# Optimization experiments

Hardware: AMD Instinct MI355X
Metric: run time of the kernel (lower is better)

The kernel has to match this reference:

```python
import jax, jax.numpy as jnp
import numpy as np

B, C, H, W = 4, 256, 48, 48
NH = 4                 # num_heads
HD = C // NH           # head_dim = 64
KD = HD // 2           # key_dim = 32 (attn_ratio=0.5)
QKV_C = C + 2 * KD * NH  # 512
FF = 2 * C             # 512
EPS = 1e-3             # ultralytics BatchNorm2d eps


def _bn(x, g, b, m, v):
    # eval-mode BatchNorm2d over channel dim 1 of NCHW
    s = g / jnp.sqrt(v + EPS)
    return x * s[:, None, None] + (b - m * s)[:, None, None]


def _conv1x1(x, w):
    # w: [out_c, in_c]
    return jnp.einsum('bchw,oc->bohw', x, w)


def _dwconv3x3(x, w):
    # depthwise 3x3, padding 1; w: [C, 1, 3, 3]
    return jax.lax.conv_general_dilated(
        x, w, (1, 1), [(1, 1), (1, 1)],
        dimension_numbers=('NCHW', 'OIHW', 'NCHW'),
        feature_group_count=C)


def setup_inputs() -> dict:
    key = jax.random.key(0)
    ks = jax.random.split(key, 32)
    d = {}
    d['x'] = jax.random.normal(ks[0], (B, C, H, W), dtype=jnp.float32)

    def bn_params(i, ch):
        g = 0.5 + jax.random.uniform(ks[i], (ch,), dtype=jnp.float32)
        b = 0.1 * jax.random.normal(ks[i + 1], (ch,), dtype=jnp.float32)
        m = 0.1 * jax.random.normal(ks[i + 2], (ch,), dtype=jnp.float32)
        v = 0.5 + jax.random.uniform(ks[i + 3], (ch,), dtype=jnp.float32)
        return g, b, m, v

    d['qkv_w'] = 0.05 * jax.random.normal(ks[1], (QKV_C, C), dtype=jnp.float32)
    d['qkv_g'], d['qkv_b'], d['qkv_m'], d['qkv_v'] = bn_params(2, QKV_C)
    d['pe_w'] = 0.1 * jax.random.normal(ks[6], (C, 1, 3, 3), dtype=jnp.float32)
    d['pe_g'], d['pe_b'], d['pe_m'], d['pe_v'] = bn_params(7, C)
    d['proj_w'] = 0.05 * jax.random.normal(ks[11], (C, C), dtype=jnp.float32)
    d['proj_g'], d['proj_b'], d['proj_m'], d['proj_v'] = bn_params(12, C)
    d['f1_w'] = 0.05 * jax.random.normal(ks[16], (FF, C), dtype=jnp.float32)
    d['f1_g'], d['f1_b'], d['f1_m'], d['f1_v'] = bn_params(17, FF)
    d['f2_w'] = 0.05 * jax.random.normal(ks[21], (C, FF), dtype=jnp.float32)
    d['f2_g'], d['f2_b'], d['f2_m'], d['f2_v'] = bn_params(22, C)
    return d


def reference(x, qkv_w, qkv_g, qkv_b, qkv_m, qkv_v,
              pe_w, pe_g, pe_b, pe_m, pe_v,
              proj_w, proj_g, proj_b, proj_m, proj_v,
              f1_w, f1_g, f1_b, f1_m, f1_v,
              f2_w, f2_g, f2_b, f2_m, f2_v):
    b, c, h, w = x.shape
    n = h * w
    # --- Attention ---
    qkv = _bn(_conv1x1(x, qkv_w), qkv_g, qkv_b, qkv_m, qkv_v)
    qkv = qkv.reshape(b, NH, 2 * KD + HD, n)
    q = qkv[:, :, :KD]            # [b, nh, kd, n]
    k = qkv[:, :, KD:2 * KD]      # [b, nh, kd, n]
    v = qkv[:, :, 2 * KD:]        # [b, nh, hd, n]
    attn = jnp.einsum('bhkn,bhkm->bhnm', q, k) * (KD ** -0.5)
    attn = jax.nn.softmax(attn, axis=-1)
    o = jnp.einsum('bhdm,bhnm->bhdn', v, attn).reshape(b, c, h, w)
    pe = _bn(_dwconv3x3(v.reshape(b, c, h, w), pe_w), pe_g, pe_b, pe_m, pe_v)
    attn_out = _bn(_conv1x1(o + pe, proj_w), proj_g, proj_b, proj_m, proj_v)
    x = x + attn_out  # shortcut
    # --- FFN ---
    f = _conv1x1(x, f1_w)
    f = _bn(f, f1_g, f1_b, f1_m, f1_v)
    f = f * jax.nn.sigmoid(f)  # SiLU
    f = _bn(_conv1x1(f, f2_w), f2_g, f2_b, f2_m, f2_v)
    return x + f  # shortcut
```

## Files before the change

kernel.cpp:

```cpp
#include <hip/hip_runtime.h>
#include <math.h>

#define Bb   4
#define Cc   256
#define Hh   48
#define Ww   48
#define NNp  2304
#define Rr   9216
#define NHd  4
#define QKVC 512
#define EPSf 1e-3f

typedef unsigned int   u32;
typedef unsigned short u16;
typedef __attribute__((ext_vector_type(8))) __bf16 bf16x8;
typedef __attribute__((ext_vector_type(4))) float  f32x4;

#if __has_builtin(__builtin_amdgcn_exp2f)
#define EXP2F(x) __builtin_amdgcn_exp2f(x)
#else
#define EXP2F(x) __expf((x) * 0.6931471805599453f)
#endif

__device__ __forceinline__ u16 f2bf(float f) {
    u32 u = __float_as_uint(f);
    u = (u + 0x7fffu + ((u >> 16) & 1u)) >> 16;
    return (u16)u;
}
__device__ __forceinline__ float bf2f(u16 h) {
    return __uint_as_float((u32)h << 16);
}
__device__ __forceinline__ u32 pk2bf(float a, float b) {
    union { __bf16 h; u16 u; } ua, ub;
    ua.h = (__bf16)a; ub.h = (__bf16)b;
    return (u32)ua.u | ((u32)ub.u << 16);
}
__device__ __forceinline__ void gload16(const void* gsrc, void* ldst) {
    __builtin_amdgcn_global_load_lds(
        (const __attribute__((address_space(1))) u32*)gsrc,
        (__attribute__((address_space(3))) u32*)ldst, 16, 0, 0);
}

__global__ __launch_bounds__(64)
void prep_all(const float* __restrict__ W0, const float* __restrict__ g0, const float* __restrict__ b0, const float* __restrict__ m0, const float* __restrict__ v0, u16* __restrict__ Wb0, float* __restrict__ bi0,
              const float* __restrict__ W1, const float* __restrict__ g1, const float* __restrict__ b1, const float* __restrict__ m1, const float* __restrict__ v1, u16* __restrict__ Wb1, float* __restrict__ bi1,
              const float* __restrict__ W2, const float* __restrict__ g2, const float* __restrict__ b2, const float* __restrict__ m2, const float* __restrict__ v2, u16* __restrict__ Wb2, float* __restrict__ bi2,
              const float* __restrict__ W3, const float* __restrict__ g3, const float* __restrict__ b3, const float* __restrict__ m3, const float* __restrict__ v3, u16* __restrict__ Wb3, float* __restrict__ bi3)
{
    const int bid = blockIdx.x;
    const float *W, *gp, *bp, *mp, *vp;
    u16* Wb; float* bias;
    int K = 256, oc;
    float c = 1.f;
    if (bid < 512) {
        oc = bid; W = W0; gp = g0; bp = b0; mp = m0; vp = v0; Wb = Wb0; bias = bi0;
        if ((oc & 127) < 32) c = 0.17677669529663687f * 1.4426950408889634f;
    } else if (bid < 768) {
        oc = bid - 512; W = W1; gp = g1; bp = b1; mp = m1; vp = v1; Wb = Wb1; bias = bi1;
    } else if (bid < 1280) {
        oc = bid - 768; W = W2; gp = g2; bp = b2; mp = m2; vp = v2; Wb = Wb2; bias = bi2;
    } else {
        oc = bid - 1280; W = W3; gp = g3; bp = b3; mp = m3; vp = v3; Wb = Wb3; bias = bi3;
        K = 512;
    }
    const int lane = threadIdx.x;
    const float s = gp[oc] * rsqrtf(vp[oc] + EPSf);
    if (lane == 0) bias[oc] = (bp[oc] - mp[oc] * s) * c;
    const float sc = s * c;
    for (int k0 = lane * 4; k0 < K; k0 += 256) {
        const float4 w = *(const float4*)(W + (size_t)oc * K + k0);
        u32 lo = (u32)f2bf(w.x * sc) | ((u32)f2bf(w.y * sc) << 16);
        u32 hi = (u32)f2bf(w.z * sc) | ((u32)f2bf(w.w * sc) << 16);
        *(uint2*)(Wb + (size_t)oc * K + k0) = make_uint2(lo, hi);
    }
}

__global__ __launch_bounds__(256)
void cvt_x(const float* __restrict__ x, u16* __restrict__ Xt)
{
    const int b = blockIdx.z, c0 = blockIdx.y * 64, n0 = blockIdx.x * 64;
    __shared__ float tile[64][65];
    const int tid = threadIdx.x;
    {
        const int n = tid & 63, cl = tid >> 6;
        #pragma unroll
        for (int cc = 0; cc < 16; ++cc) {
            const int c = cc * 4 + cl;
            tile[c][n] = x[((size_t)b * Cc + c0 + c) * NNp + n0 + n];
        }
    }
    __syncthreads();
    {
        const int n = tid >> 2, q = tid & 3;
        #pragma unroll
        for (int j = 0; j < 2; ++j) {
            const int ch = q * 2 + j, c = ch * 8;
            u32 w[4];
            #pragma unroll
            for (int e = 0; e < 4; ++e)
                w[e] = (u32)f2bf(tile[c + 2*e][n]) | ((u32)f2bf(tile[c + 2*e + 1][n]) << 16);
            *(uint4*)(Xt + ((size_t)b * NNp + n0 + n) * Cc + c0 + c)
                = make_uint4(w[0], w[1], w[2], w[3]);
        }
    }
}

template<int BN_, int FN_, int MODE>
__global__ __launch_bounds__(256)
void gemm_mfma(const u16* __restrict__ A, const u16* __restrict__ Bx,
               const float* __restrict__ bias, const float* __restrict__ resid,
               float* __restrict__ Yf, u16* __restrict__ Yt, int M, int K)
{
    constexpr int WN = FN_ * 16;
    const int r0 = blockIdx.x * BN_;
    const int m0 = blockIdx.y * 128;
    const int tid = threadIdx.x;
    const int lane = tid & 63, wid = tid >> 6;
    const int g = lane >> 4, i16 = lane & 15;
    const int wr = wid >> 1, wc = wid & 1;

    __shared__ __align__(16) u16 Al[2][4][128][8];
    __shared__ __align__(16) u16 Bl[2][4][BN_][8];

    f32x4 acc[4][FN_];
    #pragma unroll
    for (int i = 0; i < 4; ++i)
        #pragma unroll
        for (int j = 0; j < FN_; ++j) acc[i][j] = (f32x4){0.f, 0.f, 0.f, 0.f};

    #pragma unroll
    for (int ii = 0; ii < 2; ++ii) {
        const int ci = ii * 256 + tid;
        gload16(A + (size_t)(m0 + (ci & 127)) * K + (ci >> 7) * 8,
                (u16*)&Al[0][0][0][0] + (size_t)ci * 8);
    }
    if (BN_ == 128) {
        #pragma unroll
        for (int ii = 0; ii < 2; ++ii) {
            const int ci = ii * 256 + tid;
            gload16(Bx + (size_t)(r0 + (ci & 127)) * K + (ci >> 7) * 8,
                    (u16*)&Bl[0][0][0][0] + (size_t)ci * 8);
        }
    } else {
        gload16(Bx + (size_t)(r0 + (tid & 63)) * K + (tid >> 6) * 8,
                (u16*)&Bl[0][0][0][0] + (size_t)tid * 8);
    }
    __syncthreads();

    int buf = 0;
    for (int k0 = 0; k0 < K; k0 += 32) {
        if (k0 + 32 < K) {
            const int kn = k0 + 32;
            #pragma unroll
            for (int ii = 0; ii < 2; ++ii) {
                const int ci = ii * 256 + tid;
                gload16(A + (size_t)(m0 + (ci & 127)) * K + kn + (ci >> 7) * 8,
                        (u16*)&Al[buf ^ 1][0][0][0] + (size_t)ci * 8);
            }
            if (BN_ == 128) {
                #pragma unroll
                for (int ii = 0; ii < 2; ++ii) {
                    const int ci = ii * 256 + tid;
                    gload16(Bx + (size_t)(r0 + (ci & 127)) * K + kn + (ci >> 7) * 8,
                            (u16*)&Bl[buf ^ 1][0][0][0] + (size_t)ci * 8);
                }
            } else {
                gload16(Bx + (size_t)(r0 + (tid & 63)) * K + kn + (tid >> 6) * 8,
                        (u16*)&Bl[buf ^ 1][0][0][0] + (size_t)tid * 8);
            }
        }
        bf16x8 af[4], bf[FN_];
        #pragma unroll
        for (int ao = 0; ao < 4; ++ao)
            af[ao] = *(const bf16x8*)&Al[buf][g][wr * 64 + ao * 16 + i16][0];
        #pragma unroll
        for (int bo = 0; bo < FN_; ++bo)
            bf[bo] = *(const bf16x8*)&Bl[buf][g][wc * WN + bo * 16 + i16][0];
        __builtin_amdgcn_s_setprio(1);
        #pragma unroll
        for (int ao = 0; ao < 4; ++ao)
            #pragma unroll
            for (int bo = 0; bo < FN_; ++bo)
                acc[ao][bo] = __builtin_amdgcn_mfma_f32_16x16x32_bf16(
                    af[ao], bf[bo], acc[ao][bo], 0, 0, 0);
        __builtin_amdgcn_s_setprio(0);
        __syncthreads();
        buf ^= 1;
    }

    const int b  = r0 / NNp;
    const int nb = r0 - b * NNp;
    #pragma unroll
    for (int ao = 0; ao < 4; ++ao) {
        const int oc0 = m0 + wr * 64 + ao * 16 + g * 4;
        const float4 t4 = *(const float4*)(bias + oc0);
        #pragma unroll
        for (int bo = 0; bo < FN_; ++bo) {
            const int nloc = wc * WN + bo * 16 + i16;
            float y[4];
            y[0] = acc[ao][bo][0] + t4.x;  y[1] = acc[ao][bo][1] + t4.y;
            y[2] = acc[ao][bo][2] + t4.z;  y[3] = acc[ao][bo][3] + t4.w;
            if (MODE == 1 || MODE == 3) {
                const int n = nb + nloc;
                const size_t base = ((size_t)b * M + oc0) * NNp + n;
                #pragma unroll
                for (int r = 0; r < 4; ++r) {
                    y[r] += resid[base + (size_t)r * NNp];
                    Yf[base + (size_t)r * NNp] = y[r];
                }
            }
            if (MODE == 2) {
                #pragma unroll
                for (int r = 0; r < 4; ++r) y[r] = y[r] / (1.f + __expf(-y[r]));
            }
            if (MODE != 3) {
                const size_t rG = (size_t)(r0 + nloc);
                u32 lo = (u32)f2bf(y[0]) | ((u32)f2bf(y[1]) << 16);
                u32 hi = (u32)f2bf(y[2]) | ((u32)f2bf(y[3]) << 16);
                *(uint2*)(Yt + rG * M + oc0) = make_uint2(lo, hi);
            }
        }
    }
}

__global__ __launch_bounds__(256)
void repack_v(const u16* __restrict__ Yt, u16* __restrict__ Vb)
{
    const int m0 = blockIdx.x * 64;
    const int h = blockIdx.y, b = blockIdx.z;
    const int bh = b * NHd + h;
    __shared__ u16 vt[64][72];
    const int tid = threadIdx.x;
    #pragma unroll
    for (int ii = 0; ii < 2; ++ii) {
        const int mm = ii * 32 + (tid >> 3);
        const int ch = tid & 7;
        *(uint4*)&vt[mm][ch * 8] =
            *(const uint4*)(Yt + ((size_t)b * NNp + m0 + mm) * QKVC + h * 128 + 64 + ch * 8);
    }
    __syncthreads();
    const int d = tid >> 2, mq = tid & 3;
    #pragma unroll
    for (int j = 0; j < 2; ++j) {
        const int mc = mq * 2 + j;
        u32 w[4];
        #pragma unroll
        for (int e = 0; e < 4; ++e)
            w[e] = (u32)vt[mc * 8 + 2*e][d] | ((u32)vt[mc * 8 + 2*e + 1][d] << 16);
        *(uint4*)(Vb + ((size_t)bh * 64 + d) * NNp + m0 + mc * 8)
            = make_uint4(w[0], w[1], w[2], w[3]);
    }
}

__global__ __launch_bounds__(128)
void attn_mfma(const u16* __restrict__ Yt, const u16* __restrict__ Vb,
               u16* __restrict__ Ot)
{
    __shared__ __align__(16) u16 Klds[2][4][64][8];
    __shared__ __align__(16) u16 Vlds[2][64][8][8];
    __shared__ __align__(16) u32 Plds[2][16][36];

    const int tid  = threadIdx.x;
    const int wid  = tid >> 6;
    const int lane = tid & 63;
    const int g    = lane >> 4;
    const int i16  = lane & 15;

    const int wg  = blockIdx.x;
    const int swz = (wg & 7) * 144 + (wg >> 3);
    const int xq  = swz % 72;
    const int bh  = swz / 72;
    const int h   = bh & 3, b = bh >> 2;

    const size_t bG = (size_t)b * NNp;
    const u16* Vg = Vb + (size_t)bh * 64 * NNp;

    const int nq = xq * 32 + wid * 16 + i16;
    const bf16x8 qfrag = *(const bf16x8*)(Yt + (bG + nq) * QKVC + h * 128 + g * 8);

    bf16x8 ones;
    { uint4 ov = make_uint4(0x3f803f80u, 0x3f803f80u, 0x3f803f80u, 0x3f803f80u);
      ones = *(bf16x8*)&ov; }

    const f32x4 zero = {0.f, 0.f, 0.f, 0.f};
    f32x4 oacc[4];
    f32x4 lacc = zero;
    #pragma unroll
    for (int d = 0; d < 4; ++d) oacc[d] = zero;
    float m_run = -1e30f;

    #pragma unroll
    for (int ii = 0; ii < 2; ++ii) {
        const int ci = ii * 128 + tid;
        gload16(Yt + (bG + (ci & 63)) * QKVC + h * 128 + 32 + (ci >> 6) * 8,
                (u16*)&Klds[0][0][0][0] + (size_t)ci * 8);
    }
    #pragma unroll
    for (int ii = 0; ii < 4; ++ii) {
        const int idx = ii * 128 + tid;
        const int d = idx >> 3, cp = idx & 7;
        gload16(Vg + (size_t)d * NNp + (cp ^ (d & 7)) * 8,
                (u16*)&Vlds[0][0][0][0] + (size_t)idx * 8);
    }
    __syncthreads();

    int cur = 0;
    for (int t = 0; t < 36; ++t) {
        if (t < 35) {
            const int m0 = (t + 1) * 64;
            #pragma unroll
            for (int ii = 0; ii < 2; ++ii) {
                const int ci = ii * 128 + tid;
                gload16(Yt + (bG + m0 + (ci & 63)) * QKVC + h * 128 + 32 + (ci >> 6) * 8,
                        (u16*)&Klds[cur ^ 1][0][0][0] + (size_t)ci * 8);
            }
            #pragma unroll
            for (int ii = 0; ii < 4; ++ii) {
                const int idx = ii * 128 + tid;
                const int d = idx >> 3, cp = idx & 7;
                gload16(Vg + (size_t)d * NNp + m0 + (cp ^ (d & 7)) * 8,
                        (u16*)&Vlds[cur ^ 1][0][0][0] + (size_t)idx * 8);
            }
        }

        f32x4 sac[4];
        __builtin_amdgcn_s_setprio(1);
        #pragma unroll
        for (int j = 0; j < 4; ++j) {
            const bf16x8 kf = *(const bf16x8*)&Klds[cur][g][16 * j + i16][0];
            sac[j] = __builtin_amdgcn_mfma_f32_16x16x32_bf16(kf, qfrag, zero, 0, 0, 0);
        }
        __builtin_amdgcn_s_setprio(0);

        float pm = sac[0][0];
        #pragma unroll
        for (int j = 0; j < 4; ++j)
            #pragma unroll
            for (int r = 0; r < 4; ++r) pm = fmaxf(pm, sac[j][r]);
        pm = fmaxf(pm, __shfl_xor(pm, 16));
        pm = fmaxf(pm, __shfl_xor(pm, 32));

        if (!__all(pm <= m_run + 8.f)) {
            const float mn = fmaxf(m_run, pm);
            const float fc = EXP2F(m_run - mn);
            m_run = mn;
            lacc[0] *= fc; lacc[1] *= fc; lacc[2] *= fc; lacc[3] *= fc;
            #pragma unroll
            for (int d = 0; d < 4; ++d) {
                oacc[d][0] *= fc; oacc[d][1] *= fc;
                oacc[d][2] *= fc; oacc[d][3] *= fc;
            }
        }

        {
            u32* prow = &Plds[wid][i16][0];
            #pragma unroll
            for (int j = 0; j < 4; ++j) {
                const float p0 = EXP2F(sac[j][0] - m_run);
                const float p1 = EXP2F(sac[j][1] - m_run);
                const float p2 = EXP2F(sac[j][2] - m_run);
                const float p3 = EXP2F(sac[j][3] - m_run);
                *(uint2*)&prow[8 * j + 2 * g] = make_uint2(pk2bf(p0, p1), pk2bf(p2, p3));
            }
        }

        const int d7 = i16 & 7;
        __builtin_amdgcn_s_setprio(1);
        #pragma unroll
        for (int s = 0; s < 2; ++s) {
            const bf16x8 pf = *(const bf16x8*)&Plds[wid][i16][16 * s + 4 * g];
            lacc = __builtin_amdgcn_mfma_f32_16x16x32_bf16(ones, pf, lacc, 0, 0, 0);
            #pragma unroll
            for (int db = 0; db < 4; ++db) {
                const bf16x8 vf = *(const bf16x8*)&Vlds[cur][db * 16 + i16][(4 * s + g) ^ d7][0];
                oacc[db] = __builtin_amdgcn_mfma_f32_16x16x32_bf16(vf, pf, oacc[db], 0, 0, 0);
            }
        }
        __builtin_amdgcn_s_setprio(0);

        __syncthreads();
        cur ^= 1;
    }

    const float linv = 1.f / lacc[0];
    u16* ob = Ot + (bG + nq) * Cc + h * 64;
    #pragma unroll
    for (int db = 0; db < 4; ++db) {
        u32 lo = pk2bf(oacc[db][0] * linv, oacc[db][1] * linv);
        u32 hi = pk2bf(oacc[db][2] * linv, oacc[db][3] * linv);
        *(uint2*)(ob + db * 16 + g * 4) = make_uint2(lo, hi);
    }
}

__global__ __launch_bounds__(256)
void pe_bn(const u16* __restrict__ Yt, const float* __restrict__ pw,
           const float* __restrict__ gg, const float* __restrict__ bb,
           const float* __restrict__ mm, const float* __restrict__ vv,
           u16* __restrict__ Ot)
{
    const int tid = threadIdx.x;
    const int h = blockIdx.y, b = blockIdx.z;
    const int p = blockIdx.x * 32 + (tid >> 3);
    const int ch = tid & 7;
    const int c0 = h * 64 + ch * 8;
    const int yy = p / Ww, xx = p - yy * Ww;

    float acc[8];
    #pragma unroll
    for (int j = 0; j < 8; ++j) acc[j] = 0.f;

    #pragma unroll
    for (int dy = -1; dy <= 1; ++dy) {
        const int Y = yy + dy;
        if (Y < 0 || Y >= Hh) continue;
        #pragma unroll
        for (int dx = -1; dx <= 1; ++dx) {
            const int X = xx + dx;
            if (X < 0 || X >= Ww) continue;
            const uint4 raw = *(const uint4*)(Yt +
                ((size_t)b * NNp + Y * Ww + X) * QKVC + h * 128 + 64 + ch * 8);
            const u32* rw = (const u32*)&raw;
            #pragma unroll
            for (int j = 0; j < 8; ++j) {
                const u16 hv = (u16)(rw[j >> 1] >> (16 * (j & 1)));
                acc[j] += pw[(size_t)(c0 + j) * 9 + (dy + 1) * 3 + (dx + 1)] * bf2f(hv);
            }
        }
    }

    u16* dst = Ot + ((size_t)b * NNp + p) * Cc + c0;
    uint4 old = *(uint4*)dst;
    u32* ow = (u32*)&old;
    u32 res[4];
    #pragma unroll
    for (int e = 0; e < 4; ++e) {
        u16 r0, r1;
        {
            const int j = 2 * e;
            const float s = gg[c0 + j] * rsqrtf(vv[c0 + j] + EPSf);
            const float t = bb[c0 + j] - mm[c0 + j] * s;
            r0 = f2bf(bf2f((u16)(ow[e] & 0xffff)) + acc[j] * s + t);
        }
        {
            const int j = 2 * e + 1;
            const float s = gg[c0 + j] * rsqrtf(vv[c0 + j] + EPSf);
            const float t = bb[c0 + j] - mm[c0 + j] * s;
            r1 = f2bf(bf2f((u16)(ow[e] >> 16)) + acc[j] * s + t);
        }
        res[e] = (u32)r0 | ((u32)r1 << 16);
    }
    *(uint4*)dst = make_uint4(res[0], res[1], res[2], res[3]);
}

extern "C" void kernel_launch(void* const* d_in, const int* in_sizes, int n_in,
                              void* d_out, int out_size, void* d_ws, size_t ws_size,
                              hipStream_t stream)
{
    const float* x      = (const float*)d_in[0];
    const float* qkv_w  = (const float*)d_in[1];
    const float* qkv_g  = (const float*)d_in[2];
    const float* qkv_b  = (const float*)d_in[3];
    const float* qkv_m  = (const float*)d_in[4];
    const float* qkv_v  = (const float*)d_in[5];
    const float* pe_w   = (const float*)d_in[6];
    const float* pe_g   = (const float*)d_in[7];
    const float* pe_b   = (const float*)d_in[8];
    const float* pe_m   = (const float*)d_in[9];
    const float* pe_v   = (const float*)d_in[10];
    const float* proj_w = (const float*)d_in[11];
    const float* proj_g = (const float*)d_in[12];
    const float* proj_b = (const float*)d_in[13];
    const float* proj_m = (const float*)d_in[14];
    const float* proj_v = (const float*)d_in[15];
    const float* f1_w   = (const float*)d_in[16];
    const float* f1_g   = (const float*)d_in[17];
    const float* f1_b   = (const float*)d_in[18];
    const float* f1_m   = (const float*)d_in[19];
    const float* f1_v   = (const float*)d_in[20];
    const float* f2_w   = (const float*)d_in[21];
    const float* f2_g   = (const float*)d_in[22];
    const float* f2_b   = (const float*)d_in[23];
    const float* f2_m   = (const float*)d_in[24];
    const float* f2_v   = (const float*)d_in[25];

    char* wsb = (char*)d_ws;
    u16*   Yt   = (u16*)(wsb);
    u16*   Xt   = (u16*)(wsb + 9437184);
    u16*   Vb   = (u16*)(wsb + 14155776);
    u16*   Ot   = (u16*)(wsb + 18874368);
    float* x1f  = (float*)(wsb + 23592960);
    u16*   Wq   = (u16*)(wsb + 33030144);
    u16*   Wp   = (u16*)(wsb + 33292288);
    u16*   W1   = (u16*)(wsb + 33423360);
    u16*   W2   = (u16*)(wsb + 33685504);
    float* biq  = (float*)(wsb + 33947648);
    float* bip  = (float*)(wsb + 33949696);
    float* bi1  = (float*)(wsb + 33950720);
    float* bi2  = (float*)(wsb + 33952768);
    u16*   Ft   = Yt;
    u16*   X1t  = Xt;
    float* out  = (float*)d_out;

    prep_all<<<dim3(1536), dim3(64), 0, stream>>>(
        qkv_w, qkv_g, qkv_b, qkv_m, qkv_v, Wq, biq,
        proj_w, proj_g, proj_b, proj_m, proj_v, Wp, bip,
        f1_w, f1_g, f1_b, f1_m, f1_v, W1, bi1,
        f2_w, f2_g, f2_b, f2_m, f2_v, W2, bi2);
    cvt_x<<<dim3(36, 4, 4), dim3(256), 0, stream>>>(x, Xt);

    gemm_mfma<128, 4, 0><<<dim3(72, 4), dim3(256), 0, stream>>>(
        Wq, Xt, biq, nullptr, nullptr, Yt, QKVC, 256);

    repack_v<<<dim3(36, 4, 4), dim3(256), 0, stream>>>(Yt, Vb);
    attn_mfma<<<dim3(1152), dim3(128), 0, stream>>>(Yt, Vb, Ot);
    pe_bn<<<dim3(72, 4, 4), dim3(256), 0, stream>>>(Yt, pe_w, pe_g, pe_b, pe_m, pe_v, Ot);

    gemm_mfma<64, 2, 1><<<dim3(144, 2), dim3(256), 0, stream>>>(
        Wp, Ot, bip, x, x1f, X1t, Cc, 256);

    gemm_mfma<128, 4, 2><<<dim3(72, 4), dim3(256), 0, stream>>>(
        W1, X1t, bi1, nullptr, nullptr, Ft, QKVC, 256);

    gemm_mfma<64, 2, 3><<<dim3(144, 2), dim3(256), 0, stream>>>(
        W2, Ft, bi2, x1f, out, nullptr, Cc, 512);
}
```

Measured before the change: 151.7 us.

## Use 64x64 GEMM tiles, fuse prep kernels, fold PE add into attention epilogue

Replaces the 128-wide GEMM tiles with a single 64x64 tile kernel, which gives more blocks (up to 1152) for better CU occupancy on small GEMMs but lowers per-block data reuse. It merges the weight-prep and x-transpose kernels into one launch. The depthwise PE conv now runs before attention into a separate buffer, and its result is added in the attention epilogue, so Ot no longer needs a read-modify-write pass. The PE buffer reuses the x1f workspace region, which is safe only because x1f is written later.

```diff
diff --git a/kernel.cpp b/kernel.cpp
--- a/kernel.cpp
+++ b/kernel.cpp
@@ -41,46 +41,50 @@
         (__attribute__((address_space(3))) u32*)ldst, 16, 0, 0);
 }
 
-__global__ __launch_bounds__(64)
-void prep_all(const float* __restrict__ W0, const float* __restrict__ g0, const float* __restrict__ b0, const float* __restrict__ m0, const float* __restrict__ v0, u16* __restrict__ Wb0, float* __restrict__ bi0,
-              const float* __restrict__ W1, const float* __restrict__ g1, const float* __restrict__ b1, const float* __restrict__ m1, const float* __restrict__ v1, u16* __restrict__ Wb1, float* __restrict__ bi1,
-              const float* __restrict__ W2, const float* __restrict__ g2, const float* __restrict__ b2, const float* __restrict__ m2, const float* __restrict__ v2, u16* __restrict__ Wb2, float* __restrict__ bi2,
-              const float* __restrict__ W3, const float* __restrict__ g3, const float* __restrict__ b3, const float* __restrict__ m3, const float* __restrict__ v3, u16* __restrict__ Wb3, float* __restrict__ bi3)
+__global__ __launch_bounds__(256)
+void prep_fused(const float* __restrict__ W0, const float* __restrict__ g0, const float* __restrict__ b0, const float* __restrict__ m0, const float* __restrict__ v0, u16* __restrict__ Wb0, float* __restrict__ bi0,
+                const float* __restrict__ W1, const float* __restrict__ g1, const float* __restrict__ b1, const float* __restrict__ m1, const float* __restrict__ v1, u16* __restrict__ Wb1, float* __restrict__ bi1,
+                const float* __restrict__ W2, const float* __restrict__ g2, const float* __restrict__ b2, const float* __restrict__ m2, const float* __restrict__ v2, u16* __restrict__ Wb2, float* __restrict__ bi2,
+                const float* __restrict__ W3, const float* __restrict__ g3, const float* __restrict__ b3, const float* __restrict__ m3, const float* __restrict__ v3, u16* __restrict__ Wb3, float* __restrict__ bi3,
+                const float* __restrict__ x, u16* __restrict__ Xt)
 {
     const int bid = blockIdx.x;
-    const float *W, *gp, *bp, *mp, *vp;
-    u16* Wb; float* bias;
-    int K = 256, oc;
-    float c = 1.f;
-    if (bid < 512) {
-        oc = bid; W = W0; gp = g0; bp = b0; mp = m0; vp = v0; Wb = Wb0; bias = bi0;
-        if ((oc & 127) < 32) c = 0.17677669529663687f * 1.4426950408889634f;
-    } else if (bid < 768) {
-        oc = bid - 512; W = W1; gp = g1; bp = b1; mp = m1; vp = v1; Wb = Wb1; bias = bi1;
-    } else if (bid < 1280) {
-        oc = bid - 768; W = W2; gp = g2; bp = b2; mp = m2; vp = v2; Wb = Wb2; bias = bi2;
-    } else {
-        oc = bid - 1280; W = W3; gp = g3; bp = b3; mp = m3; vp = v3; Wb = Wb3; bias = bi3;
-        K = 512;
-    }
-    const int lane = threadIdx.x;
-    const float s = gp[oc] * rsqrtf(vp[oc] + EPSf);
-    if (lane == 0) bias[oc] = (bp[oc] - mp[oc] * s) * c;
-    const float sc = s * c;
-    for (int k0 = lane * 4; k0 < K; k0 += 256) {
-        const float4 w = *(const float4*)(W + (size_t)oc * K + k0);
-        u32 lo = (u32)f2bf(w.x * sc) | ((u32)f2bf(w.y * sc) << 16);
-        u32 hi = (u32)f2bf(w.z * sc) | ((u32)f2bf(w.w * sc) << 16);
-        *(uint2*)(Wb + (size_t)oc * K + k0) = make_uint2(lo, hi);
-    }
-}
-
-__global__ __launch_bounds__(256)
-void cvt_x(const float* __restrict__ x, u16* __restrict__ Xt)
-{
-    const int b = blockIdx.z, c0 = blockIdx.y * 64, n0 = blockIdx.x * 64;
+    const int tid = threadIdx.x;
+    if (bid < 384) {
+        const int row = bid * 4 + (tid >> 6);
+        const int lane = tid & 63;
+        const float *W, *gp, *bp, *mp, *vp;
+        u16* Wb; float* bias;
+        int K = 256, oc;
+        float c = 1.f;
+        if (row < 512) {
+            oc = row; W = W0; gp = g0; bp = b0; mp = m0; vp = v0; Wb = Wb0; bias = bi0;
+            if ((oc & 127) < 32) c = 0.17677669529663687f * 1.4426950408889634f;
+        } else if (row < 768) {
+            oc = row - 512; W = W1; gp = g1; bp = b1; mp = m1; vp = v1; Wb = Wb1; bias = bi1;
+        } else if (row < 1280) {
+            oc = row - 768; W = W2; gp = g2; bp = b2; mp = m2; vp = v2; Wb = Wb2; bias = bi2;
+        } else {
+            oc = row - 1280; W = W3; gp = g3; bp = b3; mp = m3; vp = v3; Wb = Wb3; bias = bi3;
+            K = 512;
+        }
+        const float s = gp[oc] * rsqrtf(vp[oc] + EPSf);
+        if (lane == 0) bias[oc] = (bp[oc] - mp[oc] * s) * c;
+        const float sc = s * c;
+        for (int k0 = lane * 4; k0 < K; k0 += 256) {
+            const float4 w = *(const float4*)(W + (size_t)oc * K + k0);
+            u32 lo = (u32)f2bf(w.x * sc) | ((u32)f2bf(w.y * sc) << 16);
+            u32 hi = (u32)f2bf(w.z * sc) | ((u32)f2bf(w.w * sc) << 16);
+            *(uint2*)(Wb + (size_t)oc * K + k0) = make_uint2(lo, hi);
+        }
+        return;
+    }
+    const int cb = bid - 384;
+    const int b  = cb / 144;
+    const int rm = cb - b * 144;
+    const int c0 = (rm / 36) * 64;
+    const int n0 = (rm % 36) * 64;
     __shared__ float tile[64][65];
-    const int tid = threadIdx.x;
     {
         const int n = tid & 63, cl = tid >> 6;
         #pragma unroll
@@ -105,84 +109,49 @@
     }
 }
 
-template<int BN_, int FN_, int MODE>
+template<int MODE>
 __global__ __launch_bounds__(256)
-void gemm_mfma(const u16* __restrict__ A, const u16* __restrict__ Bx,
-               const float* __restrict__ bias, const float* __restrict__ resid,
-               float* __restrict__ Yf, u16* __restrict__ Yt, int M, int K)
-{
-    constexpr int WN = FN_ * 16;
-    const int r0 = blockIdx.x * BN_;
-    const int m0 = blockIdx.y * 128;
+void gemm64(const u16* __restrict__ A, const u16* __restrict__ Bx,
+            const float* __restrict__ bias, const float* __restrict__ resid,
+            float* __restrict__ Yf, u16* __restrict__ Yt, int M, int K)
+{
+    const int r0 = blockIdx.x * 64;
+    const int m0 = blockIdx.y * 64;
     const int tid = threadIdx.x;
     const int lane = tid & 63, wid = tid >> 6;
     const int g = lane >> 4, i16 = lane & 15;
-    const int wr = wid >> 1, wc = wid & 1;
-
-    __shared__ __align__(16) u16 Al[2][4][128][8];
-    __shared__ __align__(16) u16 Bl[2][4][BN_][8];
-
-    f32x4 acc[4][FN_];
-    #pragma unroll
-    for (int i = 0; i < 4; ++i)
-        #pragma unroll
-        for (int j = 0; j < FN_; ++j) acc[i][j] = (f32x4){0.f, 0.f, 0.f, 0.f};
-
-    #pragma unroll
-    for (int ii = 0; ii < 2; ++ii) {
-        const int ci = ii * 256 + tid;
-        gload16(A + (size_t)(m0 + (ci & 127)) * K + (ci >> 7) * 8,
-                (u16*)&Al[0][0][0][0] + (size_t)ci * 8);
-    }
-    if (BN_ == 128) {
-        #pragma unroll
-        for (int ii = 0; ii < 2; ++ii) {
-            const int ci = ii * 256 + tid;
-            gload16(Bx + (size_t)(r0 + (ci & 127)) * K + (ci >> 7) * 8,
-                    (u16*)&Bl[0][0][0][0] + (size_t)ci * 8);
-        }
-    } else {
-        gload16(Bx + (size_t)(r0 + (tid & 63)) * K + (tid >> 6) * 8,
-                (u16*)&Bl[0][0][0][0] + (size_t)tid * 8);
-    }
+
+    __shared__ __align__(16) u16 Al[2][4][64][8];
+    __shared__ __align__(16) u16 Bl[2][4][64][8];
+
+    f32x4 acc[4];
+    #pragma unroll
+    for (int j = 0; j < 4; ++j) acc[j] = (f32x4){0.f, 0.f, 0.f, 0.f};
+
+    gload16(A + (size_t)(m0 + (tid & 63)) * K + (tid >> 6) * 8,
+            (u16*)&Al[0][0][0][0] + (size_t)tid * 8);
+    gload16(Bx + (size_t)(r0 + (tid & 63)) * K + (tid >> 6) * 8,
+            (u16*)&Bl[0][0][0][0] + (size_t)tid * 8);
     __syncthreads();
 
     int buf = 0;
     for (int k0 = 0; k0 < K; k0 += 32) {
         if (k0 + 32 < K) {
             const int kn = k0 + 32;
-            #pragma unroll
-            for (int ii = 0; ii < 2; ++ii) {
-                const int ci = ii * 256 + tid;
-                gload16(A + (size_t)(m0 + (ci & 127)) * K + kn + (ci >> 7) * 8,
-                        (u16*)&Al[buf ^ 1][0][0][0] + (size_t)ci * 8);
-            }
-            if (BN_ == 128) {
-                #pragma unroll
-                for (int ii = 0; ii < 2; ++ii) {
-                    const int ci = ii * 256 + tid;
-                    gload16(Bx + (size_t)(r0 + (ci & 127)) * K + kn + (ci >> 7) * 8,
-                            (u16*)&Bl[buf ^ 1][0][0][0] + (size_t)ci * 8);
-                }
-            } else {
-                gload16(Bx + (size_t)(r0 + (tid & 63)) * K + kn + (tid >> 6) * 8,
-                        (u16*)&Bl[buf ^ 1][0][0][0] + (size_t)tid * 8);
-            }
-        }
-        bf16x8 af[4], bf[FN_];
-        #pragma unroll
-        for (int ao = 0; ao < 4; ++ao)
-            af[ao] = *(const bf16x8*)&Al[buf][g][wr * 64 + ao * 16 + i16][0];
-        #pragma unroll
-        for (int bo = 0; bo < FN_; ++bo)
-            bf[bo] = *(const bf16x8*)&Bl[buf][g][wc * WN + bo * 16 + i16][0];
+            gload16(A + (size_t)(m0 + (tid & 63)) * K + kn + (tid >> 6) * 8,
+                    (u16*)&Al[buf ^ 1][0][0][0] + (size_t)tid * 8);
+            gload16(Bx + (size_t)(r0 + (tid & 63)) * K + kn + (tid >> 6) * 8,
+                    (u16*)&Bl[buf ^ 1][0][0][0] + (size_t)tid * 8);
+        }
+        const bf16x8 af = *(const bf16x8*)&Al[buf][g][wid * 16 + i16][0];
+        bf16x8 bf[4];
+        #pragma unroll
+        for (int bo = 0; bo < 4; ++bo)
+            bf[bo] = *(const bf16x8*)&Bl[buf][g][bo * 16 + i16][0];
         __builtin_amdgcn_s_setprio(1);
         #pragma unroll
-        for (int ao = 0; ao < 4; ++ao)
-            #pragma unroll
-            for (int bo = 0; bo < FN_; ++bo)
-                acc[ao][bo] = __builtin_amdgcn_mfma_f32_16x16x32_bf16(
-                    af[ao], bf[bo], acc[ao][bo], 0, 0, 0);
+        for (int bo = 0; bo < 4; ++bo)
+            acc[bo] = __builtin_amdgcn_mfma_f32_16x16x32_bf16(af, bf[bo], acc[bo], 0, 0, 0);
         __builtin_amdgcn_s_setprio(0);
         __syncthreads();
         buf ^= 1;
@@ -190,35 +159,30 @@
 
     const int b  = r0 / NNp;
     const int nb = r0 - b * NNp;
-    #pragma unroll
-    for (int ao = 0; ao < 4; ++ao) {
-        const int oc0 = m0 + wr * 64 + ao * 16 + g * 4;
-        const float4 t4 = *(const float4*)(bias + oc0);
-        #pragma unroll
-        for (int bo = 0; bo < FN_; ++bo) {
-            const int nloc = wc * WN + bo * 16 + i16;
-            float y[4];
-            y[0] = acc[ao][bo][0] + t4.x;  y[1] = acc[ao][bo][1] + t4.y;
-            y[2] = acc[ao][bo][2] + t4.z;  y[3] = acc[ao][bo][3] + t4.w;
-            if (MODE == 1 || MODE == 3) {
-                const int n = nb + nloc;
-                const size_t base = ((size_t)b * M + oc0) * NNp + n;
-                #pragma unroll
-                for (int r = 0; r < 4; ++r) {
-                    y[r] += resid[base + (size_t)r * NNp];
-                    Yf[base + (size_t)r * NNp] = y[r];
-                }
-            }
-            if (MODE == 2) {
-                #pragma unroll
-                for (int r = 0; r < 4; ++r) y[r] = y[r] / (1.f + __expf(-y[r]));
-            }
-            if (MODE != 3) {
-                const size_t rG = (size_t)(r0 + nloc);
-                u32 lo = (u32)f2bf(y[0]) | ((u32)f2bf(y[1]) << 16);
-                u32 hi = (u32)f2bf(y[2]) | ((u32)f2bf(y[3]) << 16);
-                *(uint2*)(Yt + rG * M + oc0) = make_uint2(lo, hi);
-            }
+    const int oc0 = m0 + wid * 16 + g * 4;
+    const float4 t4 = *(const float4*)(bias + oc0);
+    #pragma unroll
+    for (int bo = 0; bo < 4; ++bo) {
+        const int nloc = bo * 16 + i16;
+        float y[4];
+        y[0] = acc[bo][0] + t4.x;  y[1] = acc[bo][1] + t4.y;
+        y[2] = acc[bo][2] + t4.z;  y[3] = acc[bo][3] + t4.w;
+        if (MODE == 1 || MODE == 3) {
+            const int n = nb + nloc;
+            const size_t base = ((size_t)b * M + oc0) * NNp + n;
+            #pragma unroll
+            for (int r = 0; r < 4; ++r) {
+                y[r] += resid[base + (size_t)r * NNp];
+                Yf[base + (size_t)r * NNp] = y[r];
+            }
+        }
+        if (MODE == 2) {
+            #pragma unroll
+            for (int r = 0; r < 4; ++r) y[r] = y[r] / (1.f + __expf(-y[r]));
+        }
+        if (MODE != 3) {
+            const size_t rG = (size_t)(r0 + nloc);
+            *(uint2*)(Yt + rG * M + oc0) = make_uint2(pk2bf(y[0], y[1]), pk2bf(y[2], y[3]));
         }
     }
 }
@@ -252,9 +216,57 @@
     }
 }
 
+__global__ __launch_bounds__(256)
+void pe_pre(const u16* __restrict__ Yt, const float* __restrict__ pw,
+            const float* __restrict__ gg, const float* __restrict__ bb,
+            const float* __restrict__ mm, const float* __restrict__ vv,
+            u16* __restrict__ PEb)
+{
+    const int tid = threadIdx.x;
+    const int h = blockIdx.y, b = blockIdx.z;
+    const int p = blockIdx.x * 32 + (tid >> 3);
+    const int ch = tid & 7;
+    const int c0 = h * 64 + ch * 8;
+    const int yy = p / Ww, xx = p - yy * Ww;
+
+    float acc[8];
+    #pragma unroll
+    for (int j = 0; j < 8; ++j) acc[j] = 0.f;
+
+    #pragma unroll
+    for (int dy = -1; dy <= 1; ++dy) {
+        const int Y = yy + dy;
+        if (Y < 0 || Y >= Hh) continue;
+        #pragma unroll
+        for (int dx = -1; dx <= 1; ++dx) {
+            const int X = xx + dx;
+            if (X < 0 || X >= Ww) continue;
+            const uint4 raw = *(const uint4*)(Yt +
+                ((size_t)b * NNp + Y * Ww + X) * QKVC + h * 128 + 64 + ch * 8);
+            const u32* rw = (const u32*)&raw;
+            #pragma unroll
+            for (int j = 0; j < 8; ++j) {
+                const u16 hv = (u16)(rw[j >> 1] >> (16 * (j & 1)));
+                acc[j] += pw[(size_t)(c0 + j) * 9 + (dy + 1) * 3 + (dx + 1)] * bf2f(hv);
+            }
+        }
+    }
+
+    u32 res[4];
+    #pragma unroll
+    for (int e = 0; e < 4; ++e) {
+        const int j0 = 2 * e, j1 = 2 * e + 1;
+        const float s0 = gg[c0 + j0] * rsqrtf(vv[c0 + j0] + EPSf);
+        const float s1 = gg[c0 + j1] * rsqrtf(vv[c0 + j1] + EPSf);
+        res[e] = pk2bf(acc[j0] * s0 + (bb[c0 + j0] - mm[c0 + j0] * s0),
+                       acc[j1] * s1 + (bb[c0 + j1] - mm[c0 + j1] * s1));
+    }
+    *(uint4*)(PEb + ((size_t)b * NNp + p) * Cc + c0) = make_uint4(res[0], res[1], res[2], res[3]);
+}
+
 __global__ __launch_bounds__(128)
 void attn_mfma(const u16* __restrict__ Yt, const u16* __restrict__ Vb,
-               u16* __restrict__ Ot)
+               const u16* __restrict__ PEb, u16* __restrict__ Ot)
 {
     __shared__ __align__(16) u16 Klds[2][4][64][8];
     __shared__ __align__(16) u16 Vlds[2][64][8][8];
@@ -383,73 +395,17 @@
     }
 
     const float linv = 1.f / lacc[0];
+    const u16* pb = PEb + (bG + nq) * Cc + h * 64;
     u16* ob = Ot + (bG + nq) * Cc + h * 64;
     #pragma unroll
     for (int db = 0; db < 4; ++db) {
-        u32 lo = pk2bf(oacc[db][0] * linv, oacc[db][1] * linv);
-        u32 hi = pk2bf(oacc[db][2] * linv, oacc[db][3] * linv);
-        *(uint2*)(ob + db * 16 + g * 4) = make_uint2(lo, hi);
-    }
-}
-
-__global__ __launch_bounds__(256)
-void pe_bn(const u16* __restrict__ Yt, const float* __restrict__ pw,
-           const float* __restrict__ gg, const float* __restrict__ bb,
-           const float* __restrict__ mm, const float* __restrict__ vv,
-           u16* __restrict__ Ot)
-{
-    const int tid = threadIdx.x;
-    const int h = blockIdx.y, b = blockIdx.z;
-    const int p = blockIdx.x * 32 + (tid >> 3);
-    const int ch = tid & 7;
-    const int c0 = h * 64 + ch * 8;
-    const int yy = p / Ww, xx = p - yy * Ww;
-
-    float acc[8];
-    #pragma unroll
-    for (int j = 0; j < 8; ++j) acc[j] = 0.f;
-
-    #pragma unroll
-    for (int dy = -1; dy <= 1; ++dy) {
-        const int Y = yy + dy;
-        if (Y < 0 || Y >= Hh) continue;
-        #pragma unroll
-        for (int dx = -1; dx <= 1; ++dx) {
-            const int X = xx + dx;
-            if (X < 0 || X >= Ww) continue;
-            const uint4 raw = *(const uint4*)(Yt +
-                ((size_t)b * NNp + Y * Ww + X) * QKVC + h * 128 + 64 + ch * 8);
-            const u32* rw = (const u32*)&raw;
-            #pragma unroll
-            for (int j = 0; j < 8; ++j) {
-                const u16 hv = (u16)(rw[j >> 1] >> (16 * (j & 1)));
-                acc[j] += pw[(size_t)(c0 + j) * 9 + (dy + 1) * 3 + (dx + 1)] * bf2f(hv);
-            }
-        }
-    }
-
-    u16* dst = Ot + ((size_t)b * NNp + p) * Cc + c0;
-    uint4 old = *(uint4*)dst;
-    u32* ow = (u32*)&old;
-    u32 res[4];
-    #pragma unroll
-    for (int e = 0; e < 4; ++e) {
-        u16 r0, r1;
-        {
-            const int j = 2 * e;
-            const float s = gg[c0 + j] * rsqrtf(vv[c0 + j] + EPSf);
-            const float t = bb[c0 + j] - mm[c0 + j] * s;
-            r0 = f2bf(bf2f((u16)(ow[e] & 0xffff)) + acc[j] * s + t);
-        }
-        {
-            const int j = 2 * e + 1;
-            const float s = gg[c0 + j] * rsqrtf(vv[c0 + j] + EPSf);
-            const float t = bb[c0 + j] - mm[c0 + j] * s;
-            r1 = f2bf(bf2f((u16)(ow[e] >> 16)) + acc[j] * s + t);
-        }
-        res[e] = (u32)r0 | ((u32)r1 << 16);
-    }
-    *(uint4*)dst = make_uint4(res[0], res[1], res[2], res[3]);
+        const uint2 pv = *(const uint2*)(pb + db * 16 + g * 4);
+        const float y0 = oacc[db][0] * linv + bf2f((u16)(pv.x & 0xffff));
+        const float y1 = oacc[db][1] * linv + bf2f((u16)(pv.x >> 16));
+        const float y2 = oacc[db][2] * linv + bf2f((u16)(pv.y & 0xffff));
+        const float y3 = oacc[db][3] * linv + bf2f((u16)(pv.y >> 16));
+        *(uint2*)(ob + db * 16 + g * 4) = make_uint2(pk2bf(y0, y1), pk2bf(y2, y3));
+    }
 }
 
 extern "C" void kernel_launch(void* const* d_in, const int* in_sizes, int n_in,
@@ -489,6 +445,7 @@
     u16*   Vb   = (u16*)(wsb + 14155776);
     u16*   Ot   = (u16*)(wsb + 18874368);
     float* x1f  = (float*)(wsb + 23592960);
+    u16*   PEb  = (u16*)(wsb + 23592960);
     u16*   Wq   = (u16*)(wsb + 33030144);
     u16*   Wp   = (u16*)(wsb + 33292288);
     u16*   W1   = (u16*)(wsb + 33423360);
@@ -501,26 +458,26 @@
     u16*   X1t  = Xt;
     float* out  = (float*)d_out;
 
-    prep_all<<<dim3(1536), dim3(64), 0, stream>>>(
+    prep_fused<<<dim3(960), dim3(256), 0, stream>>>(
         qkv_w, qkv_g, qkv_b, qkv_m, qkv_v, Wq, biq,
         proj_w, proj_g, proj_b, proj_m, proj_v, Wp, bip,
         f1_w, f1_g, f1_b, f1_m, f1_v, W1, bi1,
-        f2_w, f2_g, f2_b, f2_m, f2_v, W2, bi2);
-    cvt_x<<<dim3(36, 4, 4), dim3(256), 0, stream>>>(x, Xt);
-
-    gemm_mfma<128, 4, 0><<<dim3(72, 4), dim3(256), 0, stream>>>(
+        f2_w, f2_g, f2_b, f2_m, f2_v, W2, bi2,
+        x, Xt);
+
+    gemm64<0><<<dim3(144, 8), dim3(256), 0, stream>>>(
         Wq, Xt, biq, nullptr, nullptr, Yt, QKVC, 256);
 
     repack_v<<<dim3(36, 4, 4), dim3(256), 0, stream>>>(Yt, Vb);
-    attn_mfma<<<dim3(1152), dim3(128), 0, stream>>>(Yt, Vb, Ot);
-    pe_bn<<<dim3(72, 4, 4), dim3(256), 0, stream>>>(Yt, pe_w, pe_g, pe_b, pe_m, pe_v, Ot);
-
-    gemm_mfma<64, 2, 1><<<dim3(144, 2), dim3(256), 0, stream>>>(
+    pe_pre<<<dim3(72, 4, 4), dim3(256), 0, stream>>>(Yt, pe_w, pe_g, pe_b, pe_m, pe_v, PEb);
+    attn_mfma<<<dim3(1152), dim3(128), 0, stream>>>(Yt, Vb, PEb, Ot);
+
+    gemm64<1><<<dim3(144, 4), dim3(256), 0, stream>>>(
         Wp, Ot, bip, x, x1f, X1t, Cc, 256);
 
-    gemm_mfma<128, 4, 2><<<dim3(72, 4), dim3(256), 0, stream>>>(
+    gemm64<2><<<dim3(144, 8), dim3(256), 0, stream>>>(
         W1, X1t, bi1, nullptr, nullptr, Ft, QKVC, 256);
 
-    gemm_mfma<64, 2, 3><<<dim3(144, 2), dim3(256), 0, stream>>>(
+    gemm64<3><<<dim3(144, 4), dim3(256), 0, stream>>>(
         W2, Ft, bi2, x1f, out, nullptr, Cc, 512);
 }
```

Result: faster. 145.3 us (-4.2%).
